# Optimization experiments

Measured on AMD Instinct MI355X. Metric: run time of the kernel, lower is better.

The kernel has to match this reference:

```python
import jax, jax.numpy as jnp
import numpy as np

EPS = 1e-8

def _gn1(x, w, b):
    # GroupNorm(num_groups=1): normalize each sample over (C, T), per-channel affine.
    mean = jnp.mean(x, axis=(1, 2), keepdims=True)
    var = jnp.mean((x - mean) ** 2, axis=(1, 2), keepdims=True)
    xn = (x - mean) * jax.lax.rsqrt(var + EPS)
    return xn * w[None, :, None] + b[None, :, None]

def _film(h, e, gw, gb, bw, bb):
    # gamma/beta: Linear -> ReLU (dropout is identity in eval), broadcast over time.
    gamma = jax.nn.relu(e @ gw.T + gb)  # [B, C]
    beta = jax.nn.relu(e @ bw.T + bb)   # [B, C]
    return gamma[:, :, None] * h + beta[:, :, None]

def setup_inputs() -> dict:
    key = jax.random.key(0)
    ks = jax.random.split(key, 16)
    B, C, T = 16, 256, 16000
    s = lambda k, shape, scale: jax.random.normal(k, shape, dtype=jnp.float32) * scale
    return {
        "x": s(ks[0], (B, C, T), 1.0),
        "cue": s(ks[1], (B, 512), 1.0),
        "gn_a_w": jnp.ones((C,), jnp.float32), "gn_a_b": jnp.zeros((C,), jnp.float32),
        "gn_n_w": jnp.ones((C,), jnp.float32), "gn_n_b": jnp.zeros((C,), jnp.float32),
        "f1g_w": s(ks[2], (C, 512), 0.04), "f1g_b": jnp.zeros((C,), jnp.float32),
        "f1b_w": s(ks[3], (C, 512), 0.04), "f1b_b": jnp.zeros((C,), jnp.float32),
        "ln1_w": jnp.ones((C,), jnp.float32), "ln1_b": jnp.zeros((C,), jnp.float32),
        "conv1_w": s(ks[4], (128, C), 0.06),
        "cds_w": s(ks[5], (256, 512), 0.04),
        "f2g_w": s(ks[6], (128, 256), 0.06), "f2g_b": jnp.zeros((128,), jnp.float32),
        "f2b_w": s(ks[7], (128, 256), 0.06), "f2b_b": jnp.zeros((128,), jnp.float32),
        "ln2_w": jnp.ones((128,), jnp.float32), "ln2_b": jnp.zeros((128,), jnp.float32),
        "conv2_w": s(ks[8], (256, 128), 0.08),
    }

def reference(x, cue, gn_a_w, gn_a_b, gn_n_w, gn_n_b, f1g_w, f1g_b, f1b_w, f1b_b,
              ln1_w, ln1_b, conv1_w, cds_w, f2g_w, f2g_b, f2b_w, f2b_b,
              ln2_w, ln2_b, conv2_w):
    x = _gn1(x, gn_a_w, gn_a_b)                 # norm_audio (GroupNorm(1, C))
    x = _gn1(x, gn_n_w, gn_n_b)                 # norm (GroupNorm(1, C))
    x = _film(x, cue, f1g_w, f1g_b, f1b_w, f1b_b) + x  # film1 + residual
    x = _gn1(x, ln1_w, ln1_b)                   # layer_norm1
    x = jnp.einsum('bct,oc->bot', x, conv1_w)   # 1x1 Conv1d, no bias -> [B,128,T]
    cue2 = jax.nn.relu(cue @ cds_w.T)           # cue_down_sample2 -> [B,256]
    x = _film(x, cue2, f2g_w, f2g_b, f2b_w, f2b_b) + x  # film2 + residual
    x = _gn1(x, ln2_w, ln2_b)                   # layer_norm2
    x = jnp.einsum('bct,oc->bot', x, conv2_w)   # 1x1 Conv1d -> [B,256,T]
    return x
```

## Files before the change

### kernel.cpp

```cpp
#include <hip/hip_runtime.h>
#include <hip/hip_bf16.h>
#include <hip/hip_fp16.h>

#define T_LEN   16000
#define NB      16
#define NTT     250
#define NTB     125
#define EPSV    1e-8f

typedef _Float16 f16x8 __attribute__((ext_vector_type(8)));
typedef float    f32x4 __attribute__((ext_vector_type(4)));

__device__ __forceinline__ ushort f2h(float f) {
    _Float16 h = (_Float16)f;
    return *(ushort*)&h;
}
__device__ __forceinline__ float f4c(const float4& v, int i) {
    return i == 0 ? v.x : i == 1 ? v.y : i == 2 ? v.z : v.w;
}
__device__ __forceinline__ void gld16(const ushort* g, ushort* l) {
    __builtin_amdgcn_global_load_lds(
        (const __attribute__((address_space(1))) uint*)g,
        (__attribute__((address_space(3))) uint*)l, 16, 0, 0);
}
__device__ __forceinline__ float waveRed64(float v) {
    #pragma unroll
    for (int m = 1; m <= 32; m <<= 1) v += __shfl_xor(v, m, 64);
    return v;
}
__device__ __forceinline__ float4 ntload4(const float* p) {
    f32x4 v = __builtin_nontemporal_load((const f32x4*)p);
    return make_float4(v[0], v[1], v[2], v[3]);
}

__device__ __forceinline__ float blockSum256(float v, float* red)
{
    #pragma unroll
    for (int off = 32; off; off >>= 1) v += __shfl_down(v, off, 64);
    __syncthreads();
    if ((threadIdx.x & 63) == 0) red[threadIdx.x >> 6] = v;
    __syncthreads();
    return red[0] + red[1] + red[2] + red[3];
}

__global__ __launch_bounds__(256) void kP1F(
    const float* __restrict__ x, ushort* __restrict__ Xp,
    float* __restrict__ sp, float* __restrict__ qp,
    const float* __restrict__ cue,
    const float* __restrict__ f1g_w, const float* __restrict__ f1g_b,
    const float* __restrict__ f1b_w, const float* __restrict__ f1b_b,
    const float* __restrict__ cds_w,
    float* __restrict__ G1, float* __restrict__ B1, float* __restrict__ CUE2)
{
    const int bid = blockIdx.x;
    const int tid = threadIdx.x;
    if (bid < 256) {
        const int c = bid;
        const int lane = tid & 63, w = tid >> 6;
        const float4 wg0 = *(const float4*)(f1g_w + c*512 + lane*8);
        const float4 wg1 = *(const float4*)(f1g_w + c*512 + lane*8 + 4);
        const float4 wb0 = *(const float4*)(f1b_w + c*512 + lane*8);
        const float4 wb1 = *(const float4*)(f1b_w + c*512 + lane*8 + 4);
        const float4 wc0 = *(const float4*)(cds_w + c*512 + lane*8);
        const float4 wc1 = *(const float4*)(cds_w + c*512 + lane*8 + 4);
        #pragma unroll
        for (int bb = 0; bb < 4; ++bb) {
            const int b = w*4 + bb;
            const float4 u0 = *(const float4*)(cue + b*512 + lane*8);
            const float4 u1 = *(const float4*)(cue + b*512 + lane*8 + 4);
            float g = 0.f, bt = 0.f, cv = 0.f;
            #pragma unroll
            for (int i = 0; i < 4; ++i) {
                g  = fmaf(f4c(u0,i), f4c(wg0,i), g);  g  = fmaf(f4c(u1,i), f4c(wg1,i), g);
                bt = fmaf(f4c(u0,i), f4c(wb0,i), bt); bt = fmaf(f4c(u1,i), f4c(wb1,i), bt);
                cv = fmaf(f4c(u0,i), f4c(wc0,i), cv); cv = fmaf(f4c(u1,i), f4c(wc1,i), cv);
            }
            g = waveRed64(g); bt = waveRed64(bt); cv = waveRed64(cv);
            if (lane == 0) {
                G1[b*256 + c]   = fmaxf(g + f1g_b[c], 0.f) + 1.f;
                B1[b*256 + c]   = fmaxf(bt + f1b_b[c], 0.f);
                CUE2[b*256 + c] = fmaxf(cv, 0.f);
            }
        }
        return;
    }

    const int pb = bid - 256;
    const int b = pb / NTT, tt = pb % NTT;
    const int t0 = tt * 64;
    const int oct = tid >> 3, j = tid & 7;

    const float* xb = x + ((size_t)(b*256 + oct*8))*T_LEN + t0;

    float s_[8], q_[8];
    uint uA[4][4], uB[4][4];

    #pragma unroll
    for (int i = 0; i < 8; ++i) {
        const float4 vA = ntload4(xb + (size_t)i*T_LEN + j*4);
        const float4 vB = ntload4(xb + (size_t)i*T_LEN + 32 + j*4);
        float s4 = vA.x + vA.y + vA.z + vA.w + vB.x + vB.y + vB.z + vB.w;
        float q4 = vA.x*vA.x + vA.y*vA.y + vA.z*vA.z + vA.w*vA.w
                 + vB.x*vB.x + vB.y*vB.y + vB.z*vB.z + vB.w*vB.w;
        s_[i] = s4; q_[i] = q4;
        #pragma unroll
        for (int k = 0; k < 4; ++k) {
            const ushort ha = f2h(f4c(vA, k));
            const ushort hb = f2h(f4c(vB, k));
            if (i & 1) {
                uA[k][i >> 1] |= ((uint)ha << 16);
                uB[k][i >> 1] |= ((uint)hb << 16);
            } else {
                uA[k][i >> 1] = (uint)ha;
                uB[k][i >> 1] = (uint)hb;
            }
        }
    }

    ushort* dst = Xp + ((size_t)(b*NTT + tt)*4 + (oct >> 3))*4096;
    const int u = oct & 7;
    #pragma unroll
    for (int k = 0; k < 4; ++k) {
        const int tA = j*4 + k;
        const int tB = 32 + j*4 + k;
        uint4 wa, wb;
        wa.x = uA[k][0]; wa.y = uA[k][1]; wa.z = uA[k][2]; wa.w = uA[k][3];
        wb.x = uB[k][0]; wb.y = uB[k][1]; wb.z = uB[k][2]; wb.w = uB[k][3];
        *(uint4*)(dst + (size_t)(tA*8 + (u ^ (tA & 7)))*8) = wa;
        *(uint4*)(dst + (size_t)(tB*8 + (u ^ (tB & 7)))*8) = wb;
    }

    #pragma unroll
    for (int i = 0; i < 8; ++i) {
        s_[i] += __shfl_xor(s_[i], 1, 8);
        s_[i] += __shfl_xor(s_[i], 2, 8);
        s_[i] += __shfl_xor(s_[i], 4, 8);
        q_[i] += __shfl_xor(q_[i], 1, 8);
        q_[i] += __shfl_xor(q_[i], 2, 8);
        q_[i] += __shfl_xor(q_[i], 4, 8);
    }
    if (j == 0) {
        float* spb = sp + ((size_t)b*NTT + tt)*256 + oct*8;
        float* qpb = qp + ((size_t)b*NTT + tt)*256 + oct*8;
        *(float4*)(spb)     = make_float4(s_[0], s_[1], s_[2], s_[3]);
        *(float4*)(spb + 4) = make_float4(s_[4], s_[5], s_[6], s_[7]);
        *(float4*)(qpb)     = make_float4(q_[0], q_[1], q_[2], q_[3]);
        *(float4*)(qpb + 4) = make_float4(q_[4], q_[5], q_[6], q_[7]);
    }
}

__global__ __launch_bounds__(256) void kR_reduce(
    const float* __restrict__ sp, const float* __restrict__ qp,
    float* __restrict__ s1, float* __restrict__ q1)
{
    const int cg = blockIdx.x, b = blockIdx.y;
    const int ci = threadIdx.x & 31, ig = threadIdx.x >> 5;
    const int c = cg*32 + ci;
    float s = 0.f, q = 0.f;
    for (int i = ig; i < NTT; i += 8) {
        s += sp[((size_t)b*NTT + i)*256 + c];
        q += qp[((size_t)b*NTT + i)*256 + c];
    }
    __shared__ float rs[8][32], rq[8][32];
    rs[ig][ci] = s; rq[ig][ci] = q;
    __syncthreads();
    if (threadIdx.x < 32) {
        float ss = 0.f, qq = 0.f;
        #pragma unroll
        for (int g = 0; g < 8; ++g) { ss += rs[g][threadIdx.x]; qq += rq[g][threadIdx.x]; }
        s1[b*256 + cg*32 + threadIdx.x] = ss;
        q1[b*256 + cg*32 + threadIdx.x] = qq;
    }
}

__global__ __launch_bounds__(256) void kM2F(
    const float* __restrict__ s1, const float* __restrict__ q1,
    const float* __restrict__ gn_a_w, const float* __restrict__ gn_a_b,
    const float* __restrict__ gn_n_w, const float* __restrict__ gn_n_b,
    const float* __restrict__ G1, const float* __restrict__ B1,
    const float* __restrict__ ln1_w, const float* __restrict__ ln1_b,
    const float* __restrict__ CUE2,
    const float* __restrict__ f2g_w, const float* __restrict__ f2g_b,
    const float* __restrict__ f2b_w, const float* __restrict__ f2b_b,
    const float* __restrict__ conv1_w,
    float* __restrict__ a4o, float* __restrict__ G2,
    float* __restrict__ E, ushort* __restrict__ Msf)
{
    const int og = blockIdx.x, b = blockIdx.y;
    const int c = threadIdx.x;
    __shared__ float red[4];
    __shared__ float sc2[256], sa4[256], sd4[256], sg2[16];

    const float sc = s1[b*256 + c];
    const float qc = q1[b*256 + c];

    const float Ninv = 1.f / (256.f * 16000.f);
    const float Tf = 16000.f;

    float S  = blockSum256(sc, red);
    float Q  = blockSum256(qc, red);
    float mu1 = S * Ninv;
    float var1 = Q * Ninv - mu1 * mu1;
    float r1 = rsqrtf(var1 + EPSV);
    float a1 = gn_a_w[c] * r1;
    float d1 = gn_a_b[c] - mu1 * r1 * gn_a_w[c];

    float S2 = blockSum256(a1*sc + Tf*d1, red);
    float Q2 = blockSum256(a1*a1*qc + 2.f*a1*d1*sc + Tf*d1*d1, red);
    float mu2 = S2 * Ninv;
    float var2 = Q2 * Ninv - mu2 * mu2;
    float r2 = rsqrtf(var2 + EPSV);
    float wn = gn_n_w[c];
    float a2 = wn * r2 * a1;
    float d2 = wn * r2 * (d1 - mu2) + gn_n_b[c];

    const float g1v = G1[b*256 + c];
    const float b1v = B1[b*256 + c];
    float a3 = g1v * a2;
    float d3 = g1v * d2 + b1v;

    float S3 = blockSum256(a3*sc + Tf*d3, red);
    float Q3 = blockSum256(a3*a3*qc + 2.f*a3*d3*sc + Tf*d3*d3, red);
    float mu3 = S3 * Ninv;
    float var3 = Q3 * Ninv - mu3 * mu3;
    float r3 = rsqrtf(var3 + EPSV);
    float w1 = ln1_w[c];
    const float a4v = w1 * r3 * a3;
    const float d4v = w1 * r3 * (d3 - mu3) + ln1_b[c];
    sa4[c] = a4v;
    sd4[c] = d4v;
    if (og == 0) a4o[b*256 + c] = a4v;
    sc2[c] = CUE2[b*256 + c];
    __syncthreads();

    const int oi = c >> 4, l16 = c & 15;
    const int o = og*16 + oi;
    float g = 0.f, bt = 0.f, ed = 0.f;
    #pragma unroll
    for (int q = 0; q < 4; ++q) {
        const int k0 = l16*16 + q*4;
        const float4 a  = *(const float4*)(f2g_w  + o*256 + k0);
        const float4 bb = *(const float4*)(f2b_w  + o*256 + k0);
        const float4 cc = *(const float4*)(conv1_w + o*256 + k0);
        const float4 u  = *(const float4*)(&sc2[k0]);
        const float4 dd = *(const float4*)(&sd4[k0]);
        #pragma unroll
        for (int i = 0; i < 4; ++i) {
            g  = fmaf(f4c(u,i),  f4c(a,i),  g);
            bt = fmaf(f4c(u,i),  f4c(bb,i), bt);
            ed = fmaf(f4c(dd,i), f4c(cc,i), ed);
        }
    }
    #pragma unroll
    for (int m = 1; m <= 8; m <<= 1) {
        g  += __shfl_xor(g, m, 16);
        bt += __shfl_xor(bt, m, 16);
        ed += __shfl_xor(ed, m, 16);
    }
    if (l16 == 0) {
        const float G2v = fmaxf(g + f2g_b[o], 0.f) + 1.f;
        const float B2v = fmaxf(bt + f2b_b[o], 0.f);
        G2[b*128 + o] = G2v;
        E[b*128 + o]  = G2v * ed + B2v;
        sg2[oi] = G2v;
    }
    __syncthreads();
    const float av = sa4[c];
    #pragma unroll
    for (int i = 0; i < 16; ++i) {
        const int oo = og*16 + i;
        Msf[((size_t)b*128 + oo)*256 + c] = f2h(sg2[i] * conv1_w[oo*256 + c] * av);
    }
}

__global__ __launch_bounds__(256) void kC_gemm(
    const ushort* __restrict__ Xp, const ushort* __restrict__ Msf,
    const float* __restrict__ E,
    float* __restrict__ q2p)
{
    const int tp = blockIdx.x, b = blockIdx.y;
    const int tid = threadIdx.x, lane = tid & 63, w = tid >> 6;
    const int sub = lane >> 4, li = lane & 15;
    const int o0 = w * 32;
    __shared__ __align__(16) ushort Bs[2][16384];

    const ushort* mp = Msf + (size_t)b*32768;

    f16x8 mf[8][2];
    #pragma unroll
    for (int ks = 0; ks < 8; ++ks) {
        const int k8 = (ks >> 1)*64 + (ks & 1)*32 + 8*sub;
        #pragma unroll
        for (int fo = 0; fo < 2; ++fo)
            mf[ks][fo] = *(const f16x8*)(mp + (size_t)(o0 + fo*16 + li)*256 + k8);
    }
    float ev[2];
    #pragma unroll
    for (int fo = 0; fo < 2; ++fo)
        ev[fo] = E[b*128 + o0 + fo*16 + li];

    const ushort* src0 = Xp + ((size_t)(b*NTT + 2*tp)*4)*4096;

    #pragma unroll
    for (int m = 0; m < 8; ++m) {
        const int off = m*2048 + w*512;
        gld16(src0 + off + lane*8, &Bs[0][off]);
    }
    __syncthreads();

    float qv[2] = {0.f, 0.f};
    #pragma unroll
    for (int tile = 0; tile < 2; ++tile) {
        if (tile == 0) {
            const ushort* src1 = src0 + 16384;
            #pragma unroll
            for (int m = 0; m < 8; ++m) {
                const int off = m*2048 + w*512;
                gld16(src1 + off + lane*8, &Bs[1][off]);
            }
        }
        f32x4 acc[4][2];
        #pragma unroll
        for (int i = 0; i < 4; ++i)
            #pragma unroll
            for (int jx = 0; jx < 2; ++jx) acc[i][jx] = (f32x4){0.f,0.f,0.f,0.f};

        #pragma unroll
        for (int ks = 0; ks < 8; ++ks) {
            const int kc = ks >> 1;
            const int uo = (ks & 1)*4 + sub;
            f16x8 xf[4];
            #pragma unroll
            for (int ft = 0; ft < 4; ++ft) {
                const int tl = ft*16 + li;
                xf[ft] = *(const f16x8*)&Bs[tile][kc*4096 + tl*64 + (uo ^ (tl & 7))*8];
            }
            #pragma unroll
            for (int fo = 0; fo < 2; ++fo)
                #pragma unroll
                for (int ft = 0; ft < 4; ++ft)
                    acc[ft][fo] = __builtin_amdgcn_mfma_f32_16x16x32_f16(xf[ft], mf[ks][fo], acc[ft][fo], 0, 0, 0);
        }

        #pragma unroll
        for (int fo = 0; fo < 2; ++fo)
            #pragma unroll
            for (int ft = 0; ft < 4; ++ft)
                #pragma unroll
                for (int r = 0; r < 4; ++r) {
                    const float z = acc[ft][fo][r] + ev[fo];
                    qv[fo] += z*z;
                }
        if (tile == 0) __syncthreads();
    }

    #pragma unroll
    for (int fo = 0; fo < 2; ++fo) {
        float q = qv[fo];
        q += __shfl_xor(q, 16, 64);
        q += __shfl_xor(q, 32, 64);
        if (sub == 0)
            q2p[((size_t)b*NTB + tp)*128 + o0 + fo*16 + li] = q;
    }
}

__global__ __launch_bounds__(256) void kD2_buildF(
    const float* __restrict__ q2p,
    const float* __restrict__ ln2_w, const float* __restrict__ ln2_b,
    const float* __restrict__ Ev,
    const float* __restrict__ a4, const float* __restrict__ G2,
    const float* __restrict__ s1,
    const float* __restrict__ conv1_w, const float* __restrict__ conv2_w,
    ushort* __restrict__ Fsf, float* __restrict__ h)
{
    const int b = blockIdx.y, pg = blockIdx.x;
    const int tid = threadIdx.x;
    __shared__ float Qs[32][128];
    __shared__ float sA2[128], sAE[128], sAS[256];
    __shared__ float rS[2], rQ[2];

    sAS[tid] = a4[b*256 + tid] * s1[b*256 + tid];
    __syncthreads();

    float s2v = 0.f, qq = 0.f;
    if (tid < 128) {
        float dot = 0.f;
        #pragma unroll 4
        for (int c4 = 0; c4 < 64; ++c4) {
            const float4 cw = *(const float4*)(conv1_w + tid*256 + c4*4);
            const float4 as = *(const float4*)(&sAS[c4*4]);
            dot = fmaf(cw.x, as.x, dot); dot = fmaf(cw.y, as.y, dot);
            dot = fmaf(cw.z, as.z, dot); dot = fmaf(cw.w, as.w, dot);
        }
        s2v = G2[b*128 + tid] * dot + 16000.f * Ev[b*128 + tid];
        for (int tb = 0; tb < NTB; ++tb)
            qq += q2p[((size_t)b*NTB + tb)*128 + tid];
        float S = s2v, Q = qq;
        #pragma unroll
        for (int off = 32; off; off >>= 1) {
            S += __shfl_down(S, off, 64);
            Q += __shfl_down(Q, off, 64);
        }
        if ((tid & 63) == 0) { rS[tid >> 6] = S; rQ[tid >> 6] = Q; }
    }
    __syncthreads();
    const float N2inv = 1.f / (128.f * 16000.f);
    const float mu  = (rS[0] + rS[1]) * N2inv;
    const float var = (rQ[0] + rQ[1]) * N2inv - mu * mu;
    const float r = rsqrtf(var + EPSV);
    if (tid < 128) {
        const float a2v = ln2_w[tid] * r;
        const float d2v = ln2_b[tid] - mu * ln2_w[tid] * r;
        sA2[tid] = a2v;
        sAE[tid] = a2v * Ev[b*128 + tid] + d2v;
    }
    __syncthreads();

    #pragma unroll
    for (int k = 0; k < 16; ++k) {
        const int idx = tid + k*256;
        const int p = idx >> 7, o = idx & 127;
        Qs[p][o] = conv2_w[(pg*32 + p)*128 + o] * sA2[o] * G2[b*128 + o];
    }
    __syncthreads();
    float acc[32];
    #pragma unroll
    for (int p = 0; p < 32; ++p) acc[p] = 0.f;
    for (int o = 0; o < 128; ++o) {
        const float mv = conv1_w[o*256 + tid];
        #pragma unroll
        for (int p = 0; p < 32; ++p) acc[p] = fmaf(Qs[p][o], mv, acc[p]);
    }
    const float a = a4[b*256 + tid];
    #pragma unroll
    for (int p = 0; p < 32; ++p) {
        const size_t idx = ((size_t)b*256 + pg*32 + p)*256 + tid;
        Fsf[idx] = f2h(acc[p] * a);
    }
    if (tid < 32) {
        const int p = pg*32 + tid;
        float hv = 0.f;
        for (int o = 0; o < 128; ++o)
            hv += conv2_w[p*128 + o] * sAE[o];
        h[b*256 + p] = hv;
    }
}

__global__ __launch_bounds__(256) void kE_gemm(
    const ushort* __restrict__ Xp, const ushort* __restrict__ Fsf,
    const float* __restrict__ h, float* __restrict__ out)
{
    const int txp = blockIdx.x;
    const int b = blockIdx.y >> 1;
    const int o_base = (blockIdx.y & 1) * 128;
    const int tid = threadIdx.x, lane = tid & 63, w = tid >> 6;
    const int sub = lane >> 4, li = lane & 15;
    const int o0 = o_base + w * 32;
    __shared__ __align__(16) ushort Bs[2][16384];

    const ushort* fp = Fsf + (size_t)b*65536;

    f16x8 ff[8][2];
    #pragma unroll
    for (int ks = 0; ks < 8; ++ks) {
        const int k8 = (ks >> 1)*64 + (ks & 1)*32 + 8*sub;
        #pragma unroll
        for (int fo = 0; fo < 2; ++fo)
            ff[ks][fo] = *(const f16x8*)(fp + (size_t)(o0 + fo*16 + li)*256 + k8);
    }
    float hv[2];
    #pragma unroll
    for (int fo = 0; fo < 2; ++fo)
        hv[fo] = h[b*256 + o0 + fo*16 + li];

    const ushort* src0 = Xp + ((size_t)(b*NTT + 2*txp)*4)*4096;

    #pragma unroll
    for (int m = 0; m < 8; ++m) {
        const int off = m*2048 + w*512;
        gld16(src0 + off + lane*8, &Bs[0][off]);
    }
    __syncthreads();

    #pragma unroll
    for (int tile = 0; tile < 2; ++tile) {
        if (tile == 0) {
            const ushort* src1 = src0 + 16384;
            #pragma unroll
            for (int m = 0; m < 8; ++m) {
                const int off = m*2048 + w*512;
                gld16(src1 + off + lane*8, &Bs[1][off]);
            }
        }
        f32x4 acc[4][2];
        #pragma unroll
        for (int i = 0; i < 4; ++i)
            #pragma unroll
            for (int jx = 0; jx < 2; ++jx) acc[i][jx] = (f32x4){0.f,0.f,0.f,0.f};

        #pragma unroll
        for (int ks = 0; ks < 8; ++ks) {
            const int kc = ks >> 1;
            const int uo = (ks & 1)*4 + sub;
            f16x8 xf[4];
            #pragma unroll
            for (int ft = 0; ft < 4; ++ft) {
                const int tl = ft*16 + li;
                xf[ft] = *(const f16x8*)&Bs[tile][kc*4096 + tl*64 + (uo ^ (tl & 7))*8];
            }
            #pragma unroll
            for (int fo = 0; fo < 2; ++fo)
                #pragma unroll
                for (int ft = 0; ft < 4; ++ft)
                    acc[ft][fo] = __builtin_amdgcn_mfma_f32_16x16x32_f16(xf[ft], ff[ks][fo], acc[ft][fo], 0, 0, 0);
        }

        const int t0 = (2*txp + tile)*64;
        #pragma unroll
        for (int fo = 0; fo < 2; ++fo) {
            const int o = o0 + fo*16 + li;
            float* obase = out + ((size_t)(b*256 + o))*T_LEN + t0;
            #pragma unroll
            for (int ft = 0; ft < 4; ++ft) {
                f32x4 v;
                v[0] = acc[ft][fo][0] + hv[fo];
                v[1] = acc[ft][fo][1] + hv[fo];
                v[2] = acc[ft][fo][2] + hv[fo];
                v[3] = acc[ft][fo][3] + hv[fo];
                __builtin_nontemporal_store(v, (f32x4*)(obase + ft*16 + sub*4));
            }
        }
        if (tile == 0) __syncthreads();
    }
}

extern "C" void kernel_launch(void* const* d_in, const int* in_sizes, int n_in,
                              void* d_out, int out_size, void* d_ws, size_t ws_size,
                              hipStream_t stream)
{
    const float* x       = (const float*)d_in[0];
    const float* cue     = (const float*)d_in[1];
    const float* gn_a_w  = (const float*)d_in[2];
    const float* gn_a_b  = (const float*)d_in[3];
    const float* gn_n_w  = (const float*)d_in[4];
    const float* gn_n_b  = (const float*)d_in[5];
    const float* f1g_w   = (const float*)d_in[6];
    const float* f1g_b   = (const float*)d_in[7];
    const float* f1b_w   = (const float*)d_in[8];
    const float* f1b_b   = (const float*)d_in[9];
    const float* ln1_w   = (const float*)d_in[10];
    const float* ln1_b   = (const float*)d_in[11];
    const float* conv1_w = (const float*)d_in[12];
    const float* cds_w   = (const float*)d_in[13];
    const float* f2g_w   = (const float*)d_in[14];
    const float* f2g_b   = (const float*)d_in[15];
    const float* f2b_w   = (const float*)d_in[16];
    const float* f2b_b   = (const float*)d_in[17];
    const float* ln2_w   = (const float*)d_in[18];
    const float* ln2_b   = (const float*)d_in[19];
    const float* conv2_w = (const float*)d_in[20];
    float* out = (float*)d_out;

    float* ws = (float*)d_ws;
    float*  sp   = ws;
    float*  qp   = ws + 1024000;
    float*  G1   = ws + 2048000;
    float*  B1   = ws + 2052096;
    float*  CUE2 = ws + 2056192;
    float*  G2   = ws + 2060288;
    float*  a4   = ws + 2062336;
    float*  E    = ws + 2066432;
    float*  h    = ws + 2068480;
    float*  s1   = ws + 2072576;
    float*  q1   = ws + 2076672;
    float*  q2p  = ws + 2080768;
    ushort* Msf  = (ushort*)(ws + 2336768);
    ushort* Fsf  = (ushort*)(ws + 2598912);
    ushort* Xp   = (ushort*)(ws + 3123200);

    kP1F<<<256 + NTT*NB, 256, 0, stream>>>(x, Xp, sp, qp,
        cue, f1g_w, f1g_b, f1b_w, f1b_b, cds_w, G1, B1, CUE2);

    kR_reduce<<<dim3(8, NB), 256, 0, stream>>>(sp, qp, s1, q1);

    kM2F<<<dim3(8, NB), 256, 0, stream>>>(s1, q1,
        gn_a_w, gn_a_b, gn_n_w, gn_n_b, G1, B1, ln1_w, ln1_b,
        CUE2, f2g_w, f2g_b, f2b_w, f2b_b, conv1_w,
        a4, G2, E, Msf);

    kC_gemm<<<dim3(NTB, NB), 256, 0, stream>>>(Xp, Msf, E, q2p);

    kD2_buildF<<<dim3(8, NB), 256, 0, stream>>>(q2p, ln2_w, ln2_b, E,
                                                a4, G2, s1, conv1_w, conv2_w,
                                                Fsf, h);

    kE_gemm<<<dim3(NTB, NB*2), 256, 0, stream>>>(Xp, Fsf, h, out);
}
```

Baseline: 264.6 us.

## Process two tile pairs per block in GEMM kernels with cross-pair prefetch

Halves the grid of kC_gemm and kE_gemm so each block handles two 128-column tile pairs, amortizing the per-block load of the weight fragments (Msf/Fsf) and keeping the double buffer busy by prefetching the next pair's first tile during the current pair's second tile. This cuts redundant weight fragment loads and block launch overhead. The cost is fewer blocks (about 1000-2000), which lowers parallelism and may leave tail imbalance, since the last block handles only one pair.

```diff
diff --git a/kernel.cpp b/kernel.cpp
--- a/kernel.cpp
+++ b/kernel.cpp
@@ -6,6 +6,7 @@
 #define NB      16
 #define NTT     250
 #define NTB     125
+#define NPG     63
 #define EPSV    1e-8f
 
 typedef _Float16 f16x8 __attribute__((ext_vector_type(8)));
@@ -278,7 +279,7 @@
     const float* __restrict__ E,
     float* __restrict__ q2p)
 {
-    const int tp = blockIdx.x, b = blockIdx.y;
+    const int p0 = blockIdx.x, b = blockIdx.y;
     const int tid = threadIdx.x, lane = tid & 63, w = tid >> 6;
     const int sub = lane >> 4, li = lane & 15;
     const int o0 = w * 32;
@@ -299,68 +300,81 @@
     for (int fo = 0; fo < 2; ++fo)
         ev[fo] = E[b*128 + o0 + fo*16 + li];
 
-    const ushort* src0 = Xp + ((size_t)(b*NTT + 2*tp)*4)*4096;
+    const int npair = (p0 + NPG < NTB) ? 2 : 1;
+
+    const ushort* srcP[2];
+    srcP[0] = Xp + ((size_t)(b*NTT + 2*p0)*4)*4096;
+    srcP[1] = Xp + ((size_t)(b*NTT + 2*(p0 + NPG))*4)*4096;
 
     #pragma unroll
     for (int m = 0; m < 8; ++m) {
         const int off = m*2048 + w*512;
-        gld16(src0 + off + lane*8, &Bs[0][off]);
-    }
-    __syncthreads();
-
-    float qv[2] = {0.f, 0.f};
-    #pragma unroll
-    for (int tile = 0; tile < 2; ++tile) {
-        if (tile == 0) {
-            const ushort* src1 = src0 + 16384;
+        gld16(srcP[0] + off + lane*8, &Bs[0][off]);
+    }
+    __syncthreads();
+
+    int buf = 0;
+    for (int pp = 0; pp < npair; ++pp) {
+        float qv[2] = {0.f, 0.f};
+        #pragma unroll
+        for (int tile = 0; tile < 2; ++tile) {
+            if (tile == 0) {
+                #pragma unroll
+                for (int m = 0; m < 8; ++m) {
+                    const int off = m*2048 + w*512;
+                    gld16(srcP[pp] + 16384 + off + lane*8, &Bs[buf^1][off]);
+                }
+            } else if (pp + 1 < npair) {
+                #pragma unroll
+                for (int m = 0; m < 8; ++m) {
+                    const int off = m*2048 + w*512;
+                    gld16(srcP[pp+1] + off + lane*8, &Bs[buf^1][off]);
+                }
+            }
+            f32x4 acc[4][2];
             #pragma unroll
-            for (int m = 0; m < 8; ++m) {
-                const int off = m*2048 + w*512;
-                gld16(src1 + off + lane*8, &Bs[1][off]);
-            }
-        }
-        f32x4 acc[4][2];
-        #pragma unroll
-        for (int i = 0; i < 4; ++i)
+            for (int i = 0; i < 4; ++i)
+                #pragma unroll
+                for (int jx = 0; jx < 2; ++jx) acc[i][jx] = (f32x4){0.f,0.f,0.f,0.f};
+
             #pragma unroll
-            for (int jx = 0; jx < 2; ++jx) acc[i][jx] = (f32x4){0.f,0.f,0.f,0.f};
-
-        #pragma unroll
-        for (int ks = 0; ks < 8; ++ks) {
-            const int kc = ks >> 1;
-            const int uo = (ks & 1)*4 + sub;
-            f16x8 xf[4];
-            #pragma unroll
-            for (int ft = 0; ft < 4; ++ft) {
-                const int tl = ft*16 + li;
-                xf[ft] = *(const f16x8*)&Bs[tile][kc*4096 + tl*64 + (uo ^ (tl & 7))*8];
-            }
+            for (int ks = 0; ks < 8; ++ks) {
+                const int kc = ks >> 1;
+                const int uo = (ks & 1)*4 + sub;
+                f16x8 xf[4];
+                #pragma unroll
+                for (int ft = 0; ft < 4; ++ft) {
+                    const int tl = ft*16 + li;
+                    xf[ft] = *(const f16x8*)&Bs[buf][kc*4096 + tl*64 + (uo ^ (tl & 7))*8];
+                }
+                #pragma unroll
+                for (int fo = 0; fo < 2; ++fo)
+                    #pragma unroll
+                    for (int ft = 0; ft < 4; ++ft)
+                        acc[ft][fo] = __builtin_amdgcn_mfma_f32_16x16x32_f16(xf[ft], mf[ks][fo], acc[ft][fo], 0, 0, 0);
+            }
+
             #pragma unroll
             for (int fo = 0; fo < 2; ++fo)
                 #pragma unroll
                 for (int ft = 0; ft < 4; ++ft)
-                    acc[ft][fo] = __builtin_amdgcn_mfma_f32_16x16x32_f16(xf[ft], mf[ks][fo], acc[ft][fo], 0, 0, 0);
-        }
-
-        #pragma unroll
-        for (int fo = 0; fo < 2; ++fo)
-            #pragma unroll
-            for (int ft = 0; ft < 4; ++ft)
-                #pragma unroll
-                for (int r = 0; r < 4; ++r) {
-                    const float z = acc[ft][fo][r] + ev[fo];
-                    qv[fo] += z*z;
-                }
-        if (tile == 0) __syncthreads();
-    }
-
-    #pragma unroll
-    for (int fo = 0; fo < 2; ++fo) {
-        float q = qv[fo];
-        q += __shfl_xor(q, 16, 64);
-        q += __shfl_xor(q, 32, 64);
-        if (sub == 0)
-            q2p[((size_t)b*NTB + tp)*128 + o0 + fo*16 + li] = q;
+                    #pragma unroll
+                    for (int r = 0; r < 4; ++r) {
+                        const float z = acc[ft][fo][r] + ev[fo];
+                        qv[fo] += z*z;
+                    }
+            if (!(pp == npair - 1 && tile == 1)) __syncthreads();
+            buf ^= 1;
+        }
+        const int pair = (pp == 0) ? p0 : p0 + NPG;
+        #pragma unroll
+        for (int fo = 0; fo < 2; ++fo) {
+            float q = qv[fo];
+            q += __shfl_xor(q, 16, 64);
+            q += __shfl_xor(q, 32, 64);
+            if (sub == 0)
+                q2p[((size_t)b*NTB + pair)*128 + o0 + fo*16 + li] = q;
+        }
     }
 }
 
@@ -450,7 +464,7 @@
     const ushort* __restrict__ Xp, const ushort* __restrict__ Fsf,
     const float* __restrict__ h, float* __restrict__ out)
 {
-    const int txp = blockIdx.x;
+    const int p0 = blockIdx.x;
     const int b = blockIdx.y >> 1;
     const int o_base = (blockIdx.y & 1) * 128;
     const int tid = threadIdx.x, lane = tid & 63, w = tid >> 6;
@@ -473,64 +487,78 @@
     for (int fo = 0; fo < 2; ++fo)
         hv[fo] = h[b*256 + o0 + fo*16 + li];
 
-    const ushort* src0 = Xp + ((size_t)(b*NTT + 2*txp)*4)*4096;
+    const int npair = (p0 + NPG < NTB) ? 2 : 1;
+
+    const ushort* srcP[2];
+    srcP[0] = Xp + ((size_t)(b*NTT + 2*p0)*4)*4096;
+    srcP[1] = Xp + ((size_t)(b*NTT + 2*(p0 + NPG))*4)*4096;
 
     #pragma unroll
     for (int m = 0; m < 8; ++m) {
         const int off = m*2048 + w*512;
-        gld16(src0 + off + lane*8, &Bs[0][off]);
-    }
-    __syncthreads();
-
-    #pragma unroll
-    for (int tile = 0; tile < 2; ++tile) {
-        if (tile == 0) {
-            const ushort* src1 = src0 + 16384;
+        gld16(srcP[0] + off + lane*8, &Bs[0][off]);
+    }
+    __syncthreads();
+
+    int buf = 0;
+    for (int pp = 0; pp < npair; ++pp) {
+        #pragma unroll
+        for (int tile = 0; tile < 2; ++tile) {
+            if (tile == 0) {
+                #pragma unroll
+                for (int m = 0; m < 8; ++m) {
+                    const int off = m*2048 + w*512;
+                    gld16(srcP[pp] + 16384 + off + lane*8, &Bs[buf^1][off]);
+                }
+            } else if (pp + 1 < npair) {
+                #pragma unroll
+                for (int m = 0; m < 8; ++m) {
+                    const int off = m*2048 + w*512;
+                    gld16(srcP[pp+1] + off + lane*8, &Bs[buf^1][off]);
+                }
+            }
+            f32x4 acc[4][2];
             #pragma unroll
-            for (int m = 0; m < 8; ++m) {
-                const int off = m*2048 + w*512;
-                gld16(src1 + off + lane*8, &Bs[1][off]);
-            }
-        }
-        f32x4 acc[4][2];
-        #pragma unroll
-        for (int i = 0; i < 4; ++i)
+            for (int i = 0; i < 4; ++i)
+                #pragma unroll
+                for (int jx = 0; jx < 2; ++jx) acc[i][jx] = (f32x4){0.f,0.f,0.f,0.f};
+
             #pragma unroll
-            for (int jx = 0; jx < 2; ++jx) acc[i][jx] = (f32x4){0.f,0.f,0.f,0.f};
-
-        #pragma unroll
-        for (int ks = 0; ks < 8; ++ks) {
-            const int kc = ks >> 1;
-            const int uo = (ks & 1)*4 + sub;
-            f16x8 xf[4];
+            for (int ks = 0; ks < 8; ++ks) {
+                const int kc = ks >> 1;
+                const int uo = (ks & 1)*4 + sub;
+                f16x8 xf[4];
+                #pragma unroll
+                for (int ft = 0; ft < 4; ++ft) {
+                    const int tl = ft*16 + li;
+                    xf[ft] = *(const f16x8*)&Bs[buf][kc*4096 + tl*64 + (uo ^ (tl & 7))*8];
+                }
+                #pragma unroll
+                for (int fo = 0; fo < 2; ++fo)
+                    #pragma unroll
+                    for (int ft = 0; ft < 4; ++ft)
+                        acc[ft][fo] = __builtin_amdgcn_mfma_f32_16x16x32_f16(xf[ft], ff[ks][fo], acc[ft][fo], 0, 0, 0);
+            }
+
+            const int pair = (pp == 0) ? p0 : p0 + NPG;
+            const int t0 = (2*pair + tile)*64;
             #pragma unroll
-            for (int ft = 0; ft < 4; ++ft) {
-                const int tl = ft*16 + li;
-                xf[ft] = *(const f16x8*)&Bs[tile][kc*4096 + tl*64 + (uo ^ (tl & 7))*8];
-            }
-            #pragma unroll
-            for (int fo = 0; fo < 2; ++fo)
-                #pragma unroll
-                for (int ft = 0; ft < 4; ++ft)
-                    acc[ft][fo] = __builtin_amdgcn_mfma_f32_16x16x32_f16(xf[ft], ff[ks][fo], acc[ft][fo], 0, 0, 0);
-        }
-
-        const int t0 = (2*txp + tile)*64;
-        #pragma unroll
-        for (int fo = 0; fo < 2; ++fo) {
-            const int o = o0 + fo*16 + li;
-            float* obase = out + ((size_t)(b*256 + o))*T_LEN + t0;
-            #pragma unroll
-            for (int ft = 0; ft < 4; ++ft) {
-                f32x4 v;
-                v[0] = acc[ft][fo][0] + hv[fo];
-                v[1] = acc[ft][fo][1] + hv[fo];
-                v[2] = acc[ft][fo][2] + hv[fo];
-                v[3] = acc[ft][fo][3] + hv[fo];
-                __builtin_nontemporal_store(v, (f32x4*)(obase + ft*16 + sub*4));
-            }
-        }
-        if (tile == 0) __syncthreads();
+            for (int fo = 0; fo < 2; ++fo) {
+                const int o = o0 + fo*16 + li;
+                float* obase = out + ((size_t)(b*256 + o))*T_LEN + t0;
+                #pragma unroll
+                for (int ft = 0; ft < 4; ++ft) {
+                    f32x4 v;
+                    v[0] = acc[ft][fo][0] + hv[fo];
+                    v[1] = acc[ft][fo][1] + hv[fo];
+                    v[2] = acc[ft][fo][2] + hv[fo];
+                    v[3] = acc[ft][fo][3] + hv[fo];
+                    __builtin_nontemporal_store(v, (f32x4*)(obase + ft*16 + sub*4));
+                }
+            }
+            if (!(pp == npair - 1 && tile == 1)) __syncthreads();
+            buf ^= 1;
+        }
     }
 }
 
@@ -588,11 +616,11 @@
         CUE2, f2g_w, f2g_b, f2b_w, f2b_b, conv1_w,
         a4, G2, E, Msf);
 
-    kC_gemm<<<dim3(NTB, NB), 256, 0, stream>>>(Xp, Msf, E, q2p);
+    kC_gemm<<<dim3(NPG, NB), 256, 0, stream>>>(Xp, Msf, E, q2p);
 
     kD2_buildF<<<dim3(8, NB), 256, 0, stream>>>(q2p, ln2_w, ln2_b, E,
                                                 a4, G2, s1, conv1_w, conv2_w,
                                                 Fsf, h);
 
-    kE_gemm<<<dim3(NTB, NB*2), 256, 0, stream>>>(Xp, Fsf, h, out);
-}
+    kE_gemm<<<dim3(NPG, NB*2), 256, 0, stream>>>(Xp, Fsf, h, out);
+}
```

New measurement: 265.2 us. No clear change (+0.2%).
